# Kernel optimization log

Hardware: AMD Instinct MI355X
Metric: run time of the kernel (lower is better)

## Reference

```python
import jax, jax.numpy as jnp
import numpy as np

HIDDEN = 2048
INTER = 5632
N_EXPERTS = 8
TOP_K = 2


def setup_inputs() -> dict:
    key = jax.random.key(0)
    ks = jax.random.split(key, 6)
    x = jax.random.normal(ks[0], (4, 2048, HIDDEN), dtype=jnp.float32)
    router_w = jax.random.normal(ks[1], (N_EXPERTS, HIDDEN), dtype=jnp.float32) * 0.02
    router_b = jnp.zeros((N_EXPERTS,), dtype=jnp.float32)
    Wg = jax.random.normal(ks[2], (N_EXPERTS, INTER, HIDDEN), dtype=jnp.float32) * 0.02
    Wu = jax.random.normal(ks[3], (N_EXPERTS, INTER, HIDDEN), dtype=jnp.float32) * 0.02
    Wd = jax.random.normal(ks[4], (N_EXPERTS, HIDDEN, INTER), dtype=jnp.float32) * 0.02
    return {"x": x, "router_w": router_w, "router_b": router_b, "Wg": Wg, "Wu": Wu, "Wd": Wd}


def reference(x, router_w, router_b, Wg, Wu, Wd):
    batch_shape = x.shape[:-1]
    xf = x.reshape(-1, HIDDEN)  # [T, H]
    T = xf.shape[0]

    # Router: softmax -> top-k -> renormalize (matches torch forward)
    logits = xf @ router_w.T + router_b            # [T, E]
    probs = jax.nn.softmax(logits, axis=-1)
    w, idx = jax.lax.top_k(probs, TOP_K)           # [T, K]
    w = w / jnp.sum(w, axis=-1, keepdims=True)

    # Dense combine weights [T, E]: zero where expert not selected.
    combine = jnp.zeros((T, N_EXPERTS), dtype=xf.dtype)
    combine = combine.at[jnp.arange(T)[:, None], idx].set(w)

    # Weighted sum of SwiGLU expert outputs (loop over fixed small E).
    out = jnp.zeros_like(xf)
    for e in range(N_EXPERTS):
        g = jax.nn.silu(xf @ Wg[e].T)              # [T, I]
        u = xf @ Wu[e].T                           # [T, I]
        h = (g * u) @ Wd[e].T                      # [T, H]
        out = out + combine[:, e:e + 1] * h
    return out.reshape(*batch_shape, HIDDEN)
```

## Files before the change

kernel.cpp:

```cpp
#include <hip/hip_runtime.h>
#include <stdint.h>

#define HID 2048
#define ITR 5632
#define NE 8
#define TT 8192
#define BM 128
#define BN 128
#define BK 64
#define MT1 64
#define NT1 44
#define NT2 16

typedef __attribute__((ext_vector_type(4))) float f4;
typedef __attribute__((ext_vector_type(8))) short s8v;
typedef __attribute__((ext_vector_type(4))) float acc4;
typedef __attribute__((ext_vector_type(4))) unsigned short u4v;
typedef __attribute__((ext_vector_type(8))) unsigned short u8v;

__device__ __forceinline__ unsigned short f2bf(float f) {
    union { float f; uint32_t u; } v; v.f = f;
    uint32_t u = v.u;
    return (unsigned short)((u + 0x7FFFu + ((u >> 16) & 1u)) >> 16);
}

__device__ __forceinline__ void gload16(const unsigned short* g, unsigned short* l) {
    __builtin_amdgcn_global_load_lds(
        (const __attribute__((address_space(1))) unsigned int*)g,
        (__attribute__((address_space(3))) unsigned int*)l, 16, 0, 0);
}

#define MFMA16(a, b, c) __builtin_amdgcn_mfma_f32_16x16x32_bf16(a, b, c, 0, 0, 0)

__global__ __launch_bounds__(256) void k_xrt(const float* __restrict__ x,
                                             const float* __restrict__ rw,
                                             const float* __restrict__ rb,
                                             unsigned short* __restrict__ xb,
                                             int* __restrict__ cnt,
                                             int* __restrict__ tokL,
                                             int* __restrict__ slotL,
                                             float* __restrict__ gateL) {
    int lane = threadIdx.x & 63;
    int wv = threadIdx.x >> 6;
    int t = blockIdx.x * 4 + wv;
    const float* xr = x + (size_t)t * HID;
    unsigned short* xo = xb + (size_t)t * HID;
    float acc[NE];
    #pragma unroll
    for (int e = 0; e < NE; ++e) acc[e] = 0.f;
    #pragma unroll
    for (int i = 0; i < 8; ++i) {
        f4 xv = *(const f4*)(xr + i * 256 + lane * 4);
        u4v o = { f2bf(xv.x), f2bf(xv.y), f2bf(xv.z), f2bf(xv.w) };
        *(u4v*)(xo + i * 256 + lane * 4) = o;
        #pragma unroll
        for (int e = 0; e < NE; ++e) {
            f4 wv4 = *(const f4*)(rw + e * HID + i * 256 + lane * 4);
            acc[e] += xv.x * wv4.x + xv.y * wv4.y + xv.z * wv4.z + xv.w * wv4.w;
        }
    }
    #pragma unroll
    for (int off = 32; off; off >>= 1)
        #pragma unroll
        for (int e = 0; e < NE; ++e) acc[e] += __shfl_xor(acc[e], off, 64);
    if (lane == 0) {
        float lg[NE];
        #pragma unroll
        for (int e = 0; e < NE; ++e) lg[e] = acc[e] + rb[e];
        int i1 = 0;
        #pragma unroll
        for (int e = 1; e < NE; ++e) if (lg[e] > lg[i1]) i1 = e;
        int i2 = -1;
        #pragma unroll
        for (int e = 0; e < NE; ++e) {
            if (e == i1) continue;
            if (i2 < 0 || lg[e] > lg[i2]) i2 = e;
        }
        float ex = __expf(lg[i2] - lg[i1]);
        float w1 = 1.f / (1.f + ex);
        float w2 = ex / (1.f + ex);
        int p = atomicAdd(&cnt[i1], 1);
        tokL[i1 * TT + p] = t; slotL[i1 * TT + p] = t * 2;     gateL[i1 * TT + p] = w1;
        p = atomicAdd(&cnt[i2], 1);
        tokL[i2 * TT + p] = t; slotL[i2 * TT + p] = t * 2 + 1; gateL[i2 * TT + p] = w2;
    }
}

#define WBLK 45056
__global__ __launch_bounds__(256) void k_cvtW(const float* __restrict__ a,
                                              const float* __restrict__ b,
                                              const float* __restrict__ c,
                                              unsigned short* __restrict__ oa,
                                              unsigned short* __restrict__ ob,
                                              unsigned short* __restrict__ oc) {
    int bb = blockIdx.x;
    const float* s; unsigned short* d;
    if (bb < WBLK)            { s = a; d = oa; }
    else if (bb < 2 * WBLK)   { s = b; d = ob; bb -= WBLK; }
    else                      { s = c; d = oc; bb -= 2 * WBLK; }
    size_t i = ((size_t)bb * 256 + threadIdx.x) * 8;
    f4 va = *(const f4*)(s + i);
    f4 vb = *(const f4*)(s + i + 4);
    u8v o;
    o[0]=f2bf(va.x); o[1]=f2bf(va.y); o[2]=f2bf(va.z); o[3]=f2bf(va.w);
    o[4]=f2bf(vb.x); o[5]=f2bf(vb.y); o[6]=f2bf(vb.z); o[7]=f2bf(vb.w);
    *(u8v*)(d + i) = o;
}

__global__ __launch_bounds__(256) void k_cvt(const float* __restrict__ src,
                                             unsigned short* __restrict__ dst) {
    size_t i = ((size_t)blockIdx.x * 256 + threadIdx.x) * 8;
    f4 a = *(const f4*)(src + i);
    f4 b = *(const f4*)(src + i + 4);
    u8v o;
    o[0]=f2bf(a.x); o[1]=f2bf(a.y); o[2]=f2bf(a.z); o[3]=f2bf(a.w);
    o[4]=f2bf(b.x); o[5]=f2bf(b.y); o[6]=f2bf(b.z); o[7]=f2bf(b.w);
    *(u8v*)(dst + i) = o;
}


__global__ __launch_bounds__(256, 2) void k_gemm1b(const unsigned short* __restrict__ xb,
                                                   const unsigned short* __restrict__ WgB,
                                                   const unsigned short* __restrict__ WuB,
                                                   const int* __restrict__ cnt,
                                                   const int* __restrict__ tokL,
                                                   const int* __restrict__ slotL,
                                                   unsigned short* __restrict__ Hb) {
    int bx = blockIdx.x;
    int e = bx / (MT1 * NT1);
    int r = bx % (MT1 * NT1);
    int mt = r / NT1, nt = r % NT1;
    int M = cnt[e];
    int m0 = mt * BM;
    if (m0 >= M) return;
    int n0 = nt * BN;

    __shared__ __align__(16) unsigned short lA[BM * BK];
    __shared__ __align__(16) unsigned short lBg[BN * BK];
    __shared__ __align__(16) unsigned short lBu[BN * BK];
    __shared__ int sTok[BM];
    __shared__ int sSlot[BM];

    int tid = threadIdx.x;
    if (tid < BM) {
        int m = m0 + tid;
        int mc = m < M ? m : M - 1;
        sTok[tid] = tokL[e * TT + mc];
        sSlot[tid] = slotL[e * TT + mc];
    }
    __syncthreads();

    int wv = tid >> 6, lane = tid & 63;
    int subrow = lane >> 3;
    int colE = ((lane & 7) ^ subrow) * 8;

    const unsigned short* aSrc[4];
    const unsigned short* gSrc[4];
    const unsigned short* uSrc[4];
    #pragma unroll
    for (int i = 0; i < 4; ++i) {
        int row = (i * 4 + wv) * 8 + subrow;
        aSrc[i] = xb + (size_t)sTok[row] * HID + colE;
        gSrc[i] = WgB + ((size_t)e * ITR + n0 + row) * HID + colE;
        uSrc[i] = WuB + ((size_t)e * ITR + n0 + row) * HID + colE;
    }

    int wm = (wv >> 1) * 64, wn = (wv & 1) * 64;
    int lr = lane & 15, lk = (lane >> 4) * 8;

    acc4 zero4 = {0.f, 0.f, 0.f, 0.f};
    acc4 ag[4][4], au[4][4];
    #pragma unroll
    for (int mi = 0; mi < 4; ++mi)
        #pragma unroll
        for (int ni = 0; ni < 4; ++ni) { ag[mi][ni] = zero4; au[mi][ni] = zero4; }

    for (int k0 = 0; k0 < HID; k0 += BK) {
        if (k0) __syncthreads();
        #pragma unroll
        for (int i = 0; i < 4; ++i) {
            gload16(aSrc[i] + k0, lA  + (i * 4 + wv) * 512);
            gload16(gSrc[i] + k0, lBg + (i * 4 + wv) * 512);
            gload16(uSrc[i] + k0, lBu + (i * 4 + wv) * 512);
        }
        __syncthreads();
        #pragma unroll
        for (int kk = 0; kk < BK; kk += 32) {
            s8v af[4], gf[4], uf[4];
            #pragma unroll
            for (int i = 0; i < 4; ++i) {
                int rowA = wm + i * 16 + lr;
                af[i] = *(const s8v*)((char*)lA + ((rowA * 128 + (kk + lk) * 2) ^ ((rowA & 7) << 4)));
                int rowB = wn + i * 16 + lr;
                int bb = (rowB * 128 + (kk + lk) * 2) ^ ((rowB & 7) << 4);
                gf[i] = *(const s8v*)((char*)lBg + bb);
                uf[i] = *(const s8v*)((char*)lBu + bb);
            }
            #pragma unroll
            for (int mi = 0; mi < 4; ++mi)
                #pragma unroll
                for (int ni = 0; ni < 4; ++ni) {
                    ag[mi][ni] = MFMA16(af[mi], gf[ni], ag[mi][ni]);
                    au[mi][ni] = MFMA16(af[mi], uf[ni], au[mi][ni]);
                }
        }
    }
    #pragma unroll
    for (int mi = 0; mi < 4; ++mi) {
        #pragma unroll
        for (int j2 = 0; j2 < 4; ++j2) {
            int m = wm + mi * 16 + (lane >> 4) * 4 + j2;
            if (m0 + m < M) {
                size_t rowOff = (size_t)sSlot[m] * ITR + n0 + wn + lr;
                #pragma unroll
                for (int ni = 0; ni < 4; ++ni) {
                    float g = ag[mi][ni][j2], u = au[mi][ni][j2];
                    float h = g * (1.f / (1.f + __expf(-g))) * u;
                    Hb[rowOff + ni * 16] = f2bf(h);
                }
            }
        }
    }
}

__global__ __launch_bounds__(256, 3) void k_gemm2b(const unsigned short* __restrict__ Hb,
                                                   const unsigned short* __restrict__ WdB,
                                                   const int* __restrict__ cnt,
                                                   const int* __restrict__ tokL,
                                                   const int* __restrict__ slotL,
                                                   const float* __restrict__ gateL,
                                                   float* __restrict__ out) {
    int bx = blockIdx.x;
    int e = bx / (MT1 * NT2);
    int r = bx % (MT1 * NT2);
    int mt = r / NT2, nt = r % NT2;
    int M = cnt[e];
    int m0 = mt * BM;
    if (m0 >= M) return;
    int n0 = nt * BN;

    __shared__ __align__(16) unsigned short lA[BM * BK];
    __shared__ __align__(16) unsigned short lB[BN * BK];
    __shared__ int sTok[BM];
    __shared__ int sSlot[BM];
    __shared__ float sGate[BM];

    int tid = threadIdx.x;
    if (tid < BM) {
        int m = m0 + tid;
        int mc = m < M ? m : M - 1;
        sTok[tid] = tokL[e * TT + mc];
        sSlot[tid] = slotL[e * TT + mc];
        sGate[tid] = gateL[e * TT + mc];
    }
    __syncthreads();

    int wv = tid >> 6, lane = tid & 63;
    int subrow = lane >> 3;
    int colE = ((lane & 7) ^ subrow) * 8;

    const unsigned short* aSrc[4];
    const unsigned short* bSrc[4];
    #pragma unroll
    for (int i = 0; i < 4; ++i) {
        int row = (i * 4 + wv) * 8 + subrow;
        aSrc[i] = Hb + (size_t)sSlot[row] * ITR + colE;
        bSrc[i] = WdB + ((size_t)e * HID + n0 + row) * ITR + colE;
    }

    int wm = (wv >> 1) * 64, wn = (wv & 1) * 64;
    int lr = lane & 15, lk = (lane >> 4) * 8;

    acc4 zero4 = {0.f, 0.f, 0.f, 0.f};
    acc4 a4[4][4];
    #pragma unroll
    for (int mi = 0; mi < 4; ++mi)
        #pragma unroll
        for (int ni = 0; ni < 4; ++ni) a4[mi][ni] = zero4;

    for (int k0 = 0; k0 < ITR; k0 += BK) {
        if (k0) __syncthreads();
        #pragma unroll
        for (int i = 0; i < 4; ++i) {
            gload16(aSrc[i] + k0, lA + (i * 4 + wv) * 512);
            gload16(bSrc[i] + k0, lB + (i * 4 + wv) * 512);
        }
        __syncthreads();
        #pragma unroll
        for (int kk = 0; kk < BK; kk += 32) {
            s8v af[4], bf[4];
            #pragma unroll
            for (int i = 0; i < 4; ++i) {
                int rowA = wm + i * 16 + lr;
                af[i] = *(const s8v*)((char*)lA + ((rowA * 128 + (kk + lk) * 2) ^ ((rowA & 7) << 4)));
                int rowB = wn + i * 16 + lr;
                bf[i] = *(const s8v*)((char*)lB + ((rowB * 128 + (kk + lk) * 2) ^ ((rowB & 7) << 4)));
            }
            #pragma unroll
            for (int mi = 0; mi < 4; ++mi)
                #pragma unroll
                for (int ni = 0; ni < 4; ++ni)
                    a4[mi][ni] = MFMA16(af[mi], bf[ni], a4[mi][ni]);
        }
    }
    #pragma unroll
    for (int mi = 0; mi < 4; ++mi) {
        #pragma unroll
        for (int j2 = 0; j2 < 4; ++j2) {
            int m = wm + mi * 16 + (lane >> 4) * 4 + j2;
            if (m0 + m < M) {
                int t = sTok[m];
                float w = sGate[m];
                float* orow = out + (size_t)t * HID + n0 + wn + lr;
                #pragma unroll
                for (int ni = 0; ni < 4; ++ni)
                    atomicAdd(orow + ni * 16, w * a4[mi][ni][j2]);
            }
        }
    }
}


__global__ __launch_bounds__(256) void k_gemm1(const unsigned short* __restrict__ xb,
                                               const float* __restrict__ Wg,
                                               const float* __restrict__ Wu,
                                               const int* __restrict__ cnt,
                                               const int* __restrict__ tokL,
                                               const int* __restrict__ slotL,
                                               unsigned short* __restrict__ Hb) {
    int bx = blockIdx.x;
    int e = bx / (MT1 * NT1);
    int r = bx % (MT1 * NT1);
    int mt = r / NT1, nt = r % NT1;
    int M = cnt[e];
    int m0 = mt * BM;
    if (m0 >= M) return;
    int n0 = nt * BN;

    __shared__ __align__(16) unsigned short lA[BM * BK];
    __shared__ __align__(16) unsigned short lBg[BN * BK];
    __shared__ __align__(16) unsigned short lBu[BN * BK];
    __shared__ int sTok[BM];
    __shared__ int sSlot[BM];

    int tid = threadIdx.x;
    if (tid < BM) {
        int m = m0 + tid;
        int mc = m < M ? m : M - 1;
        sTok[tid] = tokL[e * TT + mc];
        sSlot[tid] = slotL[e * TT + mc];
    }
    __syncthreads();

    int ar = tid >> 3, ac = tid & 7;
    const unsigned short* aP[4];
    #pragma unroll
    for (int i = 0; i < 4; ++i)
        aP[i] = xb + (size_t)sTok[ar + 32 * i] * HID + ac * 8;

    int br = tid >> 4, bc = tid & 15;
    const float* gB = Wg + ((size_t)e * ITR + n0) * HID + bc * 4;
    const float* uB = Wu + ((size_t)e * ITR + n0) * HID + bc * 4;

    int wv = tid >> 6, lane = tid & 63;
    int wm = (wv >> 1) * 64, wn = (wv & 1) * 64;
    int lr = lane & 15, lk = (lane >> 4) * 8;

    acc4 zero4 = {0.f, 0.f, 0.f, 0.f};
    acc4 ag[4][4], au[4][4];
    #pragma unroll
    for (int mi = 0; mi < 4; ++mi)
        #pragma unroll
        for (int ni = 0; ni < 4; ++ni) { ag[mi][ni] = zero4; au[mi][ni] = zero4; }

    for (int k0 = 0; k0 < HID; k0 += BK) {
        if (k0) __syncthreads();
        #pragma unroll
        for (int i = 0; i < 4; ++i) {
            int row = ar + 32 * i;
            s8v v = *(const s8v*)(aP[i] + k0);
            int byt = (row * 128 + ac * 16) ^ ((row & 7) << 4);
            *(s8v*)((char*)lA + byt) = v;
        }
        #pragma unroll
        for (int i = 0; i < 8; ++i) {
            int row = br + 16 * i;
            f4 vg = *(const f4*)(gB + (size_t)row * HID + k0);
            f4 vu = *(const f4*)(uB + (size_t)row * HID + k0);
            u4v og = { f2bf(vg.x), f2bf(vg.y), f2bf(vg.z), f2bf(vg.w) };
            u4v ou = { f2bf(vu.x), f2bf(vu.y), f2bf(vu.z), f2bf(vu.w) };
            int byt = (row * 128 + bc * 8) ^ ((row & 7) << 4);
            *(u4v*)((char*)lBg + byt) = og;
            *(u4v*)((char*)lBu + byt) = ou;
        }
        __syncthreads();
        #pragma unroll
        for (int kk = 0; kk < BK; kk += 32) {
            s8v af[4], gf[4], uf[4];
            #pragma unroll
            for (int i = 0; i < 4; ++i) {
                int rowA = wm + i * 16 + lr;
                af[i] = *(const s8v*)((char*)lA + ((rowA * 128 + (kk + lk) * 2) ^ ((rowA & 7) << 4)));
                int rowB = wn + i * 16 + lr;
                int bb = (rowB * 128 + (kk + lk) * 2) ^ ((rowB & 7) << 4);
                gf[i] = *(const s8v*)((char*)lBg + bb);
                uf[i] = *(const s8v*)((char*)lBu + bb);
            }
            #pragma unroll
            for (int mi = 0; mi < 4; ++mi)
                #pragma unroll
                for (int ni = 0; ni < 4; ++ni) {
                    ag[mi][ni] = MFMA16(af[mi], gf[ni], ag[mi][ni]);
                    au[mi][ni] = MFMA16(af[mi], uf[ni], au[mi][ni]);
                }
        }
    }
    #pragma unroll
    for (int mi = 0; mi < 4; ++mi) {
        #pragma unroll
        for (int j = 0; j < 4; ++j) {
            int m = wm + mi * 16 + (lane >> 4) * 4 + j;
            if (m0 + m < M) {
                size_t rowOff = (size_t)sSlot[m] * ITR + n0 + wn + lr;
                #pragma unroll
                for (int ni = 0; ni < 4; ++ni) {
                    float g = ag[mi][ni][j], u = au[mi][ni][j];
                    float h = g * (1.f / (1.f + __expf(-g))) * u;
                    Hb[rowOff + ni * 16] = f2bf(h);
                }
            }
        }
    }
}

__global__ __launch_bounds__(256) void k_gemm2(const unsigned short* __restrict__ Hb,
                                               const float* __restrict__ Wd,
                                               const int* __restrict__ cnt,
                                               const int* __restrict__ tokL,
                                               const int* __restrict__ slotL,
                                               const float* __restrict__ gateL,
                                               float* __restrict__ out) {
    int bx = blockIdx.x;
    int e = bx / (MT1 * NT2);
    int r = bx % (MT1 * NT2);
    int mt = r / NT2, nt = r % NT2;
    int M = cnt[e];
    int m0 = mt * BM;
    if (m0 >= M) return;
    int n0 = nt * BN;

    __shared__ __align__(16) unsigned short lA[BM * BK];
    __shared__ __align__(16) unsigned short lB[BN * BK];
    __shared__ int sTok[BM];
    __shared__ int sSlot[BM];
    __shared__ float sGate[BM];

    int tid = threadIdx.x;
    if (tid < BM) {
        int m = m0 + tid;
        int mc = m < M ? m : M - 1;
        sTok[tid] = tokL[e * TT + mc];
        sSlot[tid] = slotL[e * TT + mc];
        sGate[tid] = gateL[e * TT + mc];
    }
    __syncthreads();

    int ar = tid >> 3, ac = tid & 7;
    const unsigned short* aP[4];
    #pragma unroll
    for (int i = 0; i < 4; ++i)
        aP[i] = Hb + (size_t)sSlot[ar + 32 * i] * ITR + ac * 8;

    int br = tid >> 4, bc = tid & 15;
    const float* dB = Wd + ((size_t)e * HID + n0) * ITR + bc * 4;

    int wv = tid >> 6, lane = tid & 63;
    int wm = (wv >> 1) * 64, wn = (wv & 1) * 64;
    int lr = lane & 15, lk = (lane >> 4) * 8;

    acc4 zero4 = {0.f, 0.f, 0.f, 0.f};
    acc4 a4[4][4];
    #pragma unroll
    for (int mi = 0; mi < 4; ++mi)
        #pragma unroll
        for (int ni = 0; ni < 4; ++ni) a4[mi][ni] = zero4;

    for (int k0 = 0; k0 < ITR; k0 += BK) {
        if (k0) __syncthreads();
        #pragma unroll
        for (int i = 0; i < 4; ++i) {
            int row = ar + 32 * i;
            s8v v = *(const s8v*)(aP[i] + k0);
            int byt = (row * 128 + ac * 16) ^ ((row & 7) << 4);
            *(s8v*)((char*)lA + byt) = v;
        }
        #pragma unroll
        for (int i = 0; i < 8; ++i) {
            int row = br + 16 * i;
            f4 vd = *(const f4*)(dB + (size_t)row * ITR + k0);
            u4v od = { f2bf(vd.x), f2bf(vd.y), f2bf(vd.z), f2bf(vd.w) };
            int byt = (row * 128 + bc * 8) ^ ((row & 7) << 4);
            *(u4v*)((char*)lB + byt) = od;
        }
        __syncthreads();
        #pragma unroll
        for (int kk = 0; kk < BK; kk += 32) {
            s8v af[4], bf[4];
            #pragma unroll
            for (int i = 0; i < 4; ++i) {
                int rowA = wm + i * 16 + lr;
                af[i] = *(const s8v*)((char*)lA + ((rowA * 128 + (kk + lk) * 2) ^ ((rowA & 7) << 4)));
                int rowB = wn + i * 16 + lr;
                bf[i] = *(const s8v*)((char*)lB + ((rowB * 128 + (kk + lk) * 2) ^ ((rowB & 7) << 4)));
            }
            #pragma unroll
            for (int mi = 0; mi < 4; ++mi)
                #pragma unroll
                for (int ni = 0; ni < 4; ++ni)
                    a4[mi][ni] = MFMA16(af[mi], bf[ni], a4[mi][ni]);
        }
    }
    #pragma unroll
    for (int mi = 0; mi < 4; ++mi) {
        #pragma unroll
        for (int j = 0; j < 4; ++j) {
            int m = wm + mi * 16 + (lane >> 4) * 4 + j;
            if (m0 + m < M) {
                int t = sTok[m];
                float w = sGate[m];
                float* orow = out + (size_t)t * HID + n0 + wn + lr;
                #pragma unroll
                for (int ni = 0; ni < 4; ++ni)
                    atomicAdd(orow + ni * 16, w * a4[mi][ni][j]);
            }
        }
    }
}

extern "C" void kernel_launch(void* const* d_in, const int* in_sizes, int n_in,
                              void* d_out, int out_size, void* d_ws, size_t ws_size,
                              hipStream_t stream) {
    const float* x  = (const float*)d_in[0];
    const float* rw = (const float*)d_in[1];
    const float* rb = (const float*)d_in[2];
    const float* Wg = (const float*)d_in[3];
    const float* Wu = (const float*)d_in[4];
    const float* Wd = (const float*)d_in[5];
    float* out = (float*)d_out;
    char* ws = (char*)d_ws;

    const size_t OFF_XB   = 0;
    const size_t OFF_HB   = 33554432ull;
    const size_t OFF_TOK  = 218103808ull;
    const size_t OFF_SLOT = 218365952ull;
    const size_t OFF_GATE = 218628096ull;
    const size_t OFF_CNT  = 218890240ull;
    const size_t OFF_WG   = 218891264ull;
    const size_t OFF_WU   = 403440640ull;
    const size_t OFF_WD   = 587990016ull;
    const size_t NEED     = 772539392ull;

    unsigned short* xb   = (unsigned short*)(ws + OFF_XB);
    unsigned short* Hb   = (unsigned short*)(ws + OFF_HB);
    int*   tokL  = (int*)(ws + OFF_TOK);
    int*   slotL = (int*)(ws + OFF_SLOT);
    float* gateL = (float*)(ws + OFF_GATE);
    int*   cnt   = (int*)(ws + OFF_CNT);

    hipMemsetAsync(cnt, 0, NE * sizeof(int), stream);
    hipMemsetAsync(out, 0, (size_t)out_size * sizeof(float), stream);
    k_xrt<<<2048, 256, 0, stream>>>(x, rw, rb, xb, cnt, tokL, slotL, gateL);

    if (ws_size >= NEED) {
        unsigned short* WgB = (unsigned short*)(ws + OFF_WG);
        unsigned short* WuB = (unsigned short*)(ws + OFF_WU);
        unsigned short* WdB = (unsigned short*)(ws + OFF_WD);
        k_cvtW<<<3 * WBLK, 256, 0, stream>>>(Wg, Wu, Wd, WgB, WuB, WdB);
        k_gemm1b<<<NE * MT1 * NT1, 256, 0, stream>>>(xb, WgB, WuB, cnt, tokL, slotL, Hb);
        k_gemm2b<<<NE * MT1 * NT2, 256, 0, stream>>>(Hb, WdB, cnt, tokL, slotL, gateL, out);
    } else {
        k_gemm1<<<NE * MT1 * NT1, 256, 0, stream>>>(xb, Wg, Wu, cnt, tokL, slotL, Hb);
        k_gemm2<<<NE * MT1 * NT2, 256, 0, stream>>>(Hb, Wd, cnt, tokL, slotL, gateL, out);
    }
}
```

Before: 1.806 ms.

## Overlap Wd bf16 conversion with gemm1 using idle tiles, reorder tile mapping

Removes Wd from the standalone weight-conversion kernel. Its fp32-to-bf16 conversion now runs inside the gate/up GEMM kernel, on blocks whose M tile is beyond the expert's token count and would otherwise exit at once. Those idle blocks compute a global index over all idle tiles and grid-stride over the Wd chunks, so the conversion overlaps GEMM compute. Both GEMM kernels also switch tile mapping to make mt the fastest-varying index, which changes which blocks run together and their weight-tile reuse in cache. This relies on enough idle tiles existing, and on idle blocks not delaying real GEMM blocks.

```diff
diff --git a/kernel.cpp b/kernel.cpp
--- a/kernel.cpp
+++ b/kernel.cpp
@@ -11,6 +11,7 @@
 #define MT1 64
 #define NT1 44
 #define NT2 16
+#define WBLK 45056
 
 typedef __attribute__((ext_vector_type(4))) float f4;
 typedef __attribute__((ext_vector_type(8))) short s8v;
@@ -86,18 +87,14 @@
     }
 }
 
-#define WBLK 45056
-__global__ __launch_bounds__(256) void k_cvtW(const float* __restrict__ a,
-                                              const float* __restrict__ b,
-                                              const float* __restrict__ c,
-                                              unsigned short* __restrict__ oa,
-                                              unsigned short* __restrict__ ob,
-                                              unsigned short* __restrict__ oc) {
+__global__ __launch_bounds__(256) void k_cvtGU(const float* __restrict__ a,
+                                               const float* __restrict__ b,
+                                               unsigned short* __restrict__ oa,
+                                               unsigned short* __restrict__ ob) {
     int bb = blockIdx.x;
     const float* s; unsigned short* d;
-    if (bb < WBLK)            { s = a; d = oa; }
-    else if (bb < 2 * WBLK)   { s = b; d = ob; bb -= WBLK; }
-    else                      { s = c; d = oc; bb -= 2 * WBLK; }
+    if (bb < WBLK) { s = a; d = oa; }
+    else           { s = b; d = ob; bb -= WBLK; }
     size_t i = ((size_t)bb * 256 + threadIdx.x) * 8;
     f4 va = *(const f4*)(s + i);
     f4 vb = *(const f4*)(s + i + 4);
@@ -107,21 +104,12 @@
     *(u8v*)(d + i) = o;
 }
 
-__global__ __launch_bounds__(256) void k_cvt(const float* __restrict__ src,
-                                             unsigned short* __restrict__ dst) {
-    size_t i = ((size_t)blockIdx.x * 256 + threadIdx.x) * 8;
-    f4 a = *(const f4*)(src + i);
-    f4 b = *(const f4*)(src + i + 4);
-    u8v o;
-    o[0]=f2bf(a.x); o[1]=f2bf(a.y); o[2]=f2bf(a.z); o[3]=f2bf(a.w);
-    o[4]=f2bf(b.x); o[5]=f2bf(b.y); o[6]=f2bf(b.z); o[7]=f2bf(b.w);
-    *(u8v*)(dst + i) = o;
-}
-
 
 __global__ __launch_bounds__(256, 2) void k_gemm1b(const unsigned short* __restrict__ xb,
                                                    const unsigned short* __restrict__ WgB,
                                                    const unsigned short* __restrict__ WuB,
+                                                   const float* __restrict__ Wd,
+                                                   unsigned short* __restrict__ WdB,
                                                    const int* __restrict__ cnt,
                                                    const int* __restrict__ tokL,
                                                    const int* __restrict__ slotL,
@@ -129,10 +117,36 @@
     int bx = blockIdx.x;
     int e = bx / (MT1 * NT1);
     int r = bx % (MT1 * NT1);
-    int mt = r / NT1, nt = r % NT1;
+    int nt = r / MT1, mt = r % MT1;
     int M = cnt[e];
     int m0 = mt * BM;
-    if (m0 >= M) return;
+    int tid = threadIdx.x;
+
+    if (m0 >= M) {
+        int used = (M + BM - 1) / BM;
+        int idlePre = 0, nIdle = 0;
+        #pragma unroll
+        for (int ee = 0; ee < NE; ++ee) {
+            int ue = (cnt[ee] + BM - 1) / BM;
+            if (ue > MT1) ue = MT1;
+            int ie = MT1 - ue;
+            if (ee < e) idlePre += ie;
+            nIdle += ie;
+        }
+        int idleE = MT1 - used;
+        int myIdx = idlePre * NT1 + nt * idleE + (mt - used);
+        int stride = nIdle * NT1;
+        for (int c = myIdx; c < WBLK; c += stride) {
+            size_t i = (size_t)c * 2048 + tid * 8;
+            f4 va = *(const f4*)(Wd + i);
+            f4 vb = *(const f4*)(Wd + i + 4);
+            u8v o;
+            o[0]=f2bf(va.x); o[1]=f2bf(va.y); o[2]=f2bf(va.z); o[3]=f2bf(va.w);
+            o[4]=f2bf(vb.x); o[5]=f2bf(vb.y); o[6]=f2bf(vb.z); o[7]=f2bf(vb.w);
+            *(u8v*)(WdB + i) = o;
+        }
+        return;
+    }
     int n0 = nt * BN;
 
     __shared__ __align__(16) unsigned short lA[BM * BK];
@@ -141,7 +155,6 @@
     __shared__ int sTok[BM];
     __shared__ int sSlot[BM];
 
-    int tid = threadIdx.x;
     if (tid < BM) {
         int m = m0 + tid;
         int mc = m < M ? m : M - 1;
@@ -233,7 +246,7 @@
     int bx = blockIdx.x;
     int e = bx / (MT1 * NT2);
     int r = bx % (MT1 * NT2);
-    int mt = r / NT2, nt = r % NT2;
+    int nt = r / MT1, mt = r % MT1;
     int M = cnt[e];
     int m0 = mt * BM;
     if (m0 >= M) return;
@@ -575,8 +588,8 @@
         unsigned short* WgB = (unsigned short*)(ws + OFF_WG);
         unsigned short* WuB = (unsigned short*)(ws + OFF_WU);
         unsigned short* WdB = (unsigned short*)(ws + OFF_WD);
-        k_cvtW<<<3 * WBLK, 256, 0, stream>>>(Wg, Wu, Wd, WgB, WuB, WdB);
-        k_gemm1b<<<NE * MT1 * NT1, 256, 0, stream>>>(xb, WgB, WuB, cnt, tokL, slotL, Hb);
+        k_cvtGU<<<2 * WBLK, 256, 0, stream>>>(Wg, Wu, WgB, WuB);
+        k_gemm1b<<<NE * MT1 * NT1, 256, 0, stream>>>(xb, WgB, WuB, Wd, WdB, cnt, tokL, slotL, Hb);
         k_gemm2b<<<NE * MT1 * NT2, 256, 0, stream>>>(Hb, WdB, cnt, tokL, slotL, gateL, out);
     } else {
         k_gemm1<<<NE * MT1 * NT1, 256, 0, stream>>>(xb, Wg, Wu, cnt, tokL, slotL, Hb);
```

Result: slower. 2.696 ms (+49.3%).
